# Kernel tuning notes

Measured on AMD Instinct MI355X. Metric: run time of the kernel, lower is better.

The kernel has to match this reference:

```python
import jax, jax.numpy as jnp
import numpy as np

D_MODEL = 1024
NHEAD = 16
EPS = 1e-5


def pos_embed(x, pos):
    # Faithful, vectorized form of the sparse rotation matrix in the source.
    # Source builds rot[..., i, i+1] = sin(pos*i*omega) for even i and
    # rot[..., i, i-1] = cos(pos*i*omega) for odd i, then contracts the feature
    # dim of x against the rotation (intended einsum 'btf,btfd->btd').
    # Resulting column j: even j <- x[..., j+1]*cos(pos*(j+1)*omega),
    #                     odd  j <- x[..., j-1]*sin(pos*(j-1)*omega).
    d = x.shape[-1]
    omega = jnp.pi / d
    i_even = jnp.arange(0, d, 2, dtype=x.dtype)   # even rows -> odd output cols (sin)
    i_odd = jnp.arange(1, d, 2, dtype=x.dtype)    # odd rows  -> even output cols (cos)
    p = pos[..., None]  # (L,B,1)
    sin_part = jnp.sin(p * i_even * omega) * x[..., 0::2]  # -> odd columns
    cos_part = jnp.cos(p * i_odd * omega) * x[..., 1::2]   # -> even columns
    # interleave: even col = cos_part, odd col = sin_part
    return jnp.stack([cos_part, sin_part], axis=-1).reshape(x.shape)


def layer_norm_eps(x, w, b):
    # Source uses torch.var default (unbiased, ddof=1)
    mean = jnp.mean(x, axis=-1, keepdims=True)
    var = jnp.var(x, axis=-1, keepdims=True, ddof=1)
    return w * (x - mean) / jnp.sqrt(var + EPS) + b


def mha(q, k, v, w_qkv, b_qkv, w_o, b_o, nhead):
    L, B, E = q.shape
    S = k.shape[0]
    hd = E // nhead
    wq, wk, wv = jnp.split(w_qkv, 3, axis=0)
    bq, bk, bv = jnp.split(b_qkv, 3, axis=0)
    qp = (q @ wq.T + bq).reshape(L, B, nhead, hd).transpose(1, 2, 0, 3)  # (B,h,L,hd)
    kp = (k @ wk.T + bk).reshape(S, B, nhead, hd).transpose(1, 2, 0, 3)
    vp = (v @ wv.T + bv).reshape(S, B, nhead, hd).transpose(1, 2, 0, 3)
    scale = jnp.asarray(1.0 / np.sqrt(hd), q.dtype)
    scores = jnp.einsum('bhld,bhsd->bhls', qp, kp) * scale
    attn = jax.nn.softmax(scores, axis=-1)
    out = jnp.einsum('bhls,bhsd->bhld', attn, vp)
    out = out.transpose(2, 0, 1, 3).reshape(L, B, E) @ w_o.T + b_o
    ws = attn.mean(axis=1)  # average over heads, torch default
    return out, ws


def setup_inputs() -> dict:
    key = jax.random.key(0)
    ks = jax.random.split(key, 16)
    T, S, B, E, FF = 1024, 1024, 4, D_MODEL, 4096
    sd = 0.02
    return {
        'tgt': jax.random.normal(ks[0], (T, B, E), jnp.float32),
        'memory': jax.random.normal(ks[1], (S, B, E), jnp.float32),
        'pos': jax.random.uniform(ks[2], (S, B), jnp.float32) * S,
        'query_pos': jax.random.uniform(ks[3], (T, B), jnp.float32) * T,
        'w_qkv_self': jax.random.normal(ks[4], (3 * E, E), jnp.float32) * sd,
        'b_qkv_self': jnp.zeros((3 * E,), jnp.float32),
        'w_o_self': jax.random.normal(ks[5], (E, E), jnp.float32) * sd,
        'b_o_self': jnp.zeros((E,), jnp.float32),
        'w_qkv_cross': jax.random.normal(ks[6], (3 * E, E), jnp.float32) * sd,
        'b_qkv_cross': jnp.zeros((3 * E,), jnp.float32),
        'w_o_cross': jax.random.normal(ks[7], (E, E), jnp.float32) * sd,
        'b_o_cross': jnp.zeros((E,), jnp.float32),
        'w1': jax.random.normal(ks[8], (FF, E), jnp.float32) * sd,
        'b1': jnp.zeros((FF,), jnp.float32),
        'w2': jax.random.normal(ks[9], (E, FF), jnp.float32) * sd,
        'b2': jnp.zeros((E,), jnp.float32),
        'g1': jnp.ones((E,), jnp.float32),
        'beta1': jnp.zeros((E,), jnp.float32),
        'g2': jnp.ones((E,), jnp.float32),
        'beta2': jnp.zeros((E,), jnp.float32),
    }


def reference(tgt, memory, pos, query_pos,
              w_qkv_self, b_qkv_self, w_o_self, b_o_self,
              w_qkv_cross, b_qkv_cross, w_o_cross, b_o_cross,
              w1, b1, w2, b2, g1, beta1, g2, beta2):
    # normalize_before=False, residual=True, dropout inactive (eval)
    qk = pos_embed(tgt, query_pos)
    tgt2, _ = mha(qk, qk, tgt, w_qkv_self, b_qkv_self, w_o_self, b_o_self, NHEAD)
    tgt = tgt + tgt2
    tgt = layer_norm_eps(tgt, g1, beta1)
    tgt2, ws = mha(pos_embed(tgt, query_pos), pos_embed(memory, pos), memory,
                   w_qkv_cross, b_qkv_cross, w_o_cross, b_o_cross, NHEAD)
    tgt = tgt + tgt2
    tgt = layer_norm_eps(tgt, g2, beta2)
    tgt2 = jax.nn.relu(tgt @ w1.T + b1) @ w2.T + b2
    tgt = tgt + tgt2
    return tgt, ws
```

## Files before the change

kernel.cpp:

```cpp
#include <hip/hip_runtime.h>

typedef unsigned short u16;
typedef __attribute__((ext_vector_type(8))) short short8;
typedef __attribute__((ext_vector_type(8))) unsigned short u16x8;
typedef __attribute__((ext_vector_type(4))) float f32x4;

#define GLOAD16(SRC, DST) __builtin_amdgcn_global_load_lds( \
    (const __attribute__((address_space(1))) void*)(SRC),   \
    (__attribute__((address_space(3))) void*)(DST), 16, 0, 0)

#define SWZ(BKv, r) ((BKv) == 32 ? (((r) >> 1) & 3) : ((r) & 7))

#define QSCALE 0.18033688011112042f

__device__ __forceinline__ u16 f2bf(float f) {
  union { float f; unsigned u; } v; v.f = f;
  unsigned r = v.u + 0x7fffu + ((v.u >> 16) & 1u);
  return (u16)(r >> 16);
}
__device__ __forceinline__ float bf2f(u16 h) {
  union { unsigned u; float f; } v; v.u = ((unsigned)h) << 16;
  return v.f;
}

__global__ __launch_bounds__(256) void wcvt_kernel(const float* __restrict__ s0,
                                                   const float* __restrict__ s1,
                                                   const float* __restrict__ s2,
                                                   const float* __restrict__ s3,
                                                   const float* __restrict__ s4,
                                                   const float* __restrict__ s5,
                                                   u16* __restrict__ dst) {
  long i = ((long)blockIdx.x * 256 + threadIdx.x) * 4;
  const float* src; long off;
  if (i < 3145728)        { src = s0; off = 0; }
  else if (i < 4194304)   { src = s1; off = 3145728; }
  else if (i < 7340032)   { src = s2; off = 4194304; }
  else if (i < 8388608)   { src = s3; off = 7340032; }
  else if (i < 12582912)  { src = s4; off = 8388608; }
  else                    { src = s5; off = 12582912; }
  float4 v = *(const float4*)(src + (i - off));
  ushort4 o; o.x = f2bf(v.x); o.y = f2bf(v.y); o.z = f2bf(v.z); o.w = f2bf(v.w);
  *(ushort4*)(dst + i) = o;
}

__global__ __launch_bounds__(256) void pos_embed_kernel(const float* __restrict__ x,
                                                        const float* __restrict__ pos,
                                                        u16* __restrict__ out,
                                                        u16* __restrict__ out2,
                                                        u16* __restrict__ raw) {
  int m = blockIdx.x;
  int tid = threadIdx.x;
  float p = pos[m];
  long base = ((long)m << 10);
  int j = tid * 4;
  float4 xv = *(const float4*)(x + base + j);
  const float inv = 1.0f / 2048.0f;
  float r0 = p * (float)(j + 0) * inv;
  float r1 = p * (float)(j + 1) * inv;
  float r2 = p * (float)(j + 2) * inv;
  float r3 = p * (float)(j + 3) * inv;
  float s1 = __builtin_amdgcn_sinf(r0 - floorf(r0));
  float c0 = __builtin_amdgcn_cosf(r1 - floorf(r1));
  float s3 = __builtin_amdgcn_sinf(r2 - floorf(r2));
  float c2 = __builtin_amdgcn_cosf(r3 - floorf(r3));
  ushort4 o;
  o.x = f2bf(c0 * xv.y);
  o.y = f2bf(s1 * xv.x);
  o.z = f2bf(c2 * xv.w);
  o.w = f2bf(s3 * xv.z);
  *(ushort4*)(out + base + j) = o;
  if (out2) *(ushort4*)(out2 + base + j) = o;
  if (raw) {
    ushort4 rw; rw.x = f2bf(xv.x); rw.y = f2bf(xv.y); rw.z = f2bf(xv.z); rw.w = f2bf(xv.w);
    *(ushort4*)(raw + base + j) = rw;
  }
}

__global__ __launch_bounds__(256) void split_qkv_kernel(const u16* __restrict__ P,
                                                        u16* __restrict__ Qb,
                                                        u16* __restrict__ Kb,
                                                        u16* __restrict__ Vtb) {
  long e = ((long)blockIdx.x * 256 + threadIdx.x) * 8;
  int m = (int)(e / 3072);
  int n = (int)(e % 3072);
  int t = m >> 2, b = m & 3;
  int sec = n >> 10, nn = n & 1023;
  int h = nn >> 6, d = nn & 63;
  long bh = b * 16 + h;
  u16x8 v = *(const u16x8*)(P + e);
  if (sec == 0) {
    *(u16x8*)(Qb + (bh << 16) + ((long)t << 6) + d) = v;
  } else if (sec == 1) {
    *(u16x8*)(Kb + (bh << 16) + ((long)t << 6) + d) = v;
  } else {
    u16* dst = Vtb + (bh << 16) + ((long)d << 10) + t;
#pragma unroll
    for (int q = 0; q < 8; q++) dst[(long)q << 10] = v[q];
  }
}

__global__ __launch_bounds__(256) void fattn_kernel(const u16* __restrict__ Q,
                                                    const u16* __restrict__ K,
                                                    const u16* __restrict__ Vt,
                                                    u16* __restrict__ AO,
                                                    float2* __restrict__ Ml) {
  __shared__ u16 lK[2][4096];
  __shared__ u16 lV[2][4096];
  __shared__ u16 lP[4][1024];
  const int tid = threadIdx.x, lane = tid & 63, wid = tid >> 6;
  const int nb = gridDim.x * gridDim.y;
  const int orig = blockIdx.y * gridDim.x + blockIdx.x;
  const int swz = (orig & 7) * (nb >> 3) + (orig >> 3);
  const int qt = swz & 15;
  const int bh = swz >> 4;
  const int b = bh >> 4, h = bh & 15;
  const u16* Qp = Q + ((long)bh << 16);
  const u16* Kp = K + ((long)bh << 16);
  const u16* Vp = Vt + ((long)bh << 16);
  const int q0 = qt << 6;
  const int cr = lane >> 4;

  short8 af0, af1;
  {
    const u16* qs = Qp + (long)(q0 + wid * 16 + (lane & 15)) * 64 + cr * 8;
    af0 = *(const short8*)qs;
    af1 = *(const short8*)(qs + 32);
  }

  float m = -1e30f, l = 0.f;
  f32x4 acco[4] = {};

  auto stage = [&](int bufi, int kv) {
    int s0 = kv << 6;
#pragma unroll
    for (int it = 0; it < 2; it++) {
      int c = it * 256 + tid;
      int row = c >> 3, ch = c & 7;
      int sch = (ch ^ (row & 7)) * 8;
      GLOAD16(Kp + (long)(s0 + row) * 64 + sch, &lK[bufi][c * 8]);
      GLOAD16(Vp + (long)row * 1024 + s0 + sch, &lV[bufi][c * 8]);
    }
  };

  stage(0, 0);
  __syncthreads();
  int buf = 0;
  for (int kv = 0; kv < 16; kv++) {
    if (kv < 15) stage(buf ^ 1, kv + 1);
    f32x4 accs[4];
    __builtin_amdgcn_s_setprio(1);
#pragma unroll
    for (int j = 0; j < 4; j++) {
      int sr = j * 16 + (lane & 15);
      const short8 kf0 = *(const short8*)&lK[buf][sr * 64 + ((cr ^ (sr & 7)) * 8)];
      const short8 kf1 = *(const short8*)&lK[buf][sr * 64 + (((4 + cr) ^ (sr & 7)) * 8)];
      f32x4 zz = {};
      zz = __builtin_amdgcn_mfma_f32_16x16x32_bf16(kf0, af0, zz, 0, 0, 0);
      accs[j] = __builtin_amdgcn_mfma_f32_16x16x32_bf16(kf1, af1, zz, 0, 0, 0);
    }
    __builtin_amdgcn_s_setprio(0);
    float tm = fmaxf(fmaxf(fmaxf(accs[0][0], accs[0][1]), fmaxf(accs[0][2], accs[0][3])),
                     fmaxf(fmaxf(accs[1][0], accs[1][1]), fmaxf(accs[1][2], accs[1][3])));
    float tm2 = fmaxf(fmaxf(fmaxf(accs[2][0], accs[2][1]), fmaxf(accs[2][2], accs[2][3])),
                      fmaxf(fmaxf(accs[3][0], accs[3][1]), fmaxf(accs[3][2], accs[3][3])));
    tm = fmaxf(tm, tm2);
    tm = fmaxf(tm, __shfl_xor(tm, 16));
    tm = fmaxf(tm, __shfl_xor(tm, 32));
    if (!__all(tm - m <= 8.0f)) {
      float mn = fmaxf(m, tm);
      float f = __builtin_amdgcn_exp2f(m - mn);
      m = mn; l *= f;
#pragma unroll
      for (int r = 0; r < 4; r++) {
        float fr = __shfl(f, cr * 4 + r);
        acco[0][r] *= fr; acco[1][r] *= fr; acco[2][r] *= fr; acco[3][r] *= fr;
      }
    }
    float rs = 0.f;
#pragma unroll
    for (int j = 0; j < 4; j++)
#pragma unroll
      for (int r = 0; r < 4; r++) {
        float p = __builtin_amdgcn_exp2f(accs[j][r] - m);
        accs[j][r] = p;
        rs += p;
      }
    rs += __shfl_xor(rs, 16);
    rs += __shfl_xor(rs, 32);
    l += rs;
    {
      u16* pw = lP[wid];
      int q = lane & 15;
      int rowoff = q * 64;
      int qs7 = q & 7;
#pragma unroll
      for (int j = 0; j < 4; j++) {
        uint2 pk;
        asm("v_cvt_pk_bf16_f32 %0, %1, %2"
            : "=v"(pk.x) : "v"(accs[j][0]), "v"(accs[j][1]));
        asm("v_cvt_pk_bf16_f32 %0, %1, %2"
            : "=v"(pk.y) : "v"(accs[j][2]), "v"(accs[j][3]));
        int chunk = 2 * j + (cr >> 1);
        int idx = rowoff + ((chunk ^ qs7) * 8) + 4 * (cr & 1);
        *(uint2*)(pw + idx) = pk;
      }
    }
    {
      int ql = lane & 15;
      const u16* pr = &lP[wid][ql * 64];
      short8 pa0 = *(const short8*)&pr[(cr ^ (ql & 7)) * 8];
      short8 pa1 = *(const short8*)&pr[((4 + cr) ^ (ql & 7)) * 8];
      __builtin_amdgcn_s_setprio(1);
#pragma unroll
      for (int j = 0; j < 4; j++) {
        int dr = j * 16 + (lane & 15);
        const short8 vf0 = *(const short8*)&lV[buf][dr * 64 + ((cr ^ (dr & 7)) * 8)];
        const short8 vf1 = *(const short8*)&lV[buf][dr * 64 + (((4 + cr) ^ (dr & 7)) * 8)];
        acco[j] = __builtin_amdgcn_mfma_f32_16x16x32_bf16(pa0, vf0, acco[j], 0, 0, 0);
        acco[j] = __builtin_amdgcn_mfma_f32_16x16x32_bf16(pa1, vf1, acco[j], 0, 0, 0);
      }
      __builtin_amdgcn_s_setprio(0);
    }
    __syncthreads();
    buf ^= 1;
  }
  float invl = 1.0f / l;
  float ilr[4];
#pragma unroll
  for (int r = 0; r < 4; r++) ilr[r] = __shfl(invl, cr * 4 + r);
#pragma unroll
  for (int j = 0; j < 4; j++)
#pragma unroll
    for (int r = 0; r < 4; r++) {
      int t = q0 + wid * 16 + cr * 4 + r;
      int e = (b << 10) + (h << 6) + j * 16 + (lane & 15);
      AO[(long)t * 4096 + e] = f2bf(acco[j][r] * ilr[r]);
    }
  if (Ml && lane < 16) {
    int t = q0 + wid * 16 + lane;
    Ml[((long)bh << 10) + t] = make_float2(m, invl);
  }
}

__global__ __launch_bounds__(256) void wsrec_kernel(const u16* __restrict__ Q,
                                                    const u16* __restrict__ K,
                                                    const float2* __restrict__ Ml,
                                                    float* __restrict__ ws) {
  __shared__ u16 lK[2][4096];
  const int tid = threadIdx.x, lane = tid & 63, wid = tid >> 6;
  const int nb = gridDim.x * gridDim.y;
  const int orig = blockIdx.y * gridDim.x + blockIdx.x;
  const int swz = (orig & 7) * (nb >> 3) + (orig >> 3);
  const int st = swz & 15, lt = swz >> 4;
  const int b = blockIdx.z;
  const int s0 = st << 6, l0 = lt << 6;
  const int cr = lane >> 4;

  auto stage = [&](int bufi, int h) {
    const u16* Kp = K + (((long)(b * 16 + h)) << 16);
#pragma unroll
    for (int it = 0; it < 2; it++) {
      int c = it * 256 + tid;
      int row = c >> 3, ch = c & 7;
      GLOAD16(Kp + (long)(s0 + row) * 64 + ((ch ^ (row & 7)) * 8), &lK[bufi][c * 8]);
    }
  };

  f32x4 wacc[4] = {};
  stage(0, 0);
  __syncthreads();
  int buf = 0;
  for (int h = 0; h < 16; h++) {
    if (h < 15) stage(buf ^ 1, h + 1);
    const int bh = b * 16 + h;
    short8 af0, af1;
    {
      const u16* qs = Q + ((long)bh << 16) + (long)(l0 + wid * 16 + (lane & 15)) * 64 + cr * 8;
      af0 = *(const short8*)qs;
      af1 = *(const short8*)(qs + 32);
    }
    f32x4 accs[4];
    __builtin_amdgcn_s_setprio(1);
#pragma unroll
    for (int j = 0; j < 4; j++) {
      int sr = j * 16 + (lane & 15);
      const short8 kf0 = *(const short8*)&lK[buf][sr * 64 + ((cr ^ (sr & 7)) * 8)];
      const short8 kf1 = *(const short8*)&lK[buf][sr * 64 + (((4 + cr) ^ (sr & 7)) * 8)];
      f32x4 zz = {};
      zz = __builtin_amdgcn_mfma_f32_16x16x32_bf16(af0, kf0, zz, 0, 0, 0);
      accs[j] = __builtin_amdgcn_mfma_f32_16x16x32_bf16(af1, kf1, zz, 0, 0, 0);
    }
    __builtin_amdgcn_s_setprio(0);
    float mm[4], il[4];
#pragma unroll
    for (int r = 0; r < 4; r++) {
      float2 v = Ml[((long)bh << 10) + l0 + wid * 16 + (lane >> 4) * 4 + r];
      mm[r] = v.x; il[r] = v.y * 0.0625f;
    }
#pragma unroll
    for (int j = 0; j < 4; j++)
#pragma unroll
      for (int r = 0; r < 4; r++)
        wacc[j][r] += __builtin_amdgcn_exp2f(accs[j][r] - mm[r]) * il[r];
    __syncthreads();
    buf ^= 1;
  }
#pragma unroll
  for (int j = 0; j < 4; j++)
#pragma unroll
    for (int r = 0; r < 4; r++) {
      int li = l0 + wid * 16 + (lane >> 4) * 4 + r;
      int si = s0 + j * 16 + (lane & 15);
      ws[((long)b << 20) + (long)li * 1024 + si] = wacc[j][r];
    }
}

__global__ __launch_bounds__(256) void ln_kernel(const float* __restrict__ X,
                                                 const float* __restrict__ D1,
                                                 const float* __restrict__ D2,
                                                 const float* __restrict__ bo,
                                                 const float* __restrict__ g,
                                                 const float* __restrict__ be,
                                                 float* __restrict__ out,
                                                 u16* __restrict__ bfout) {
  int mrow = blockIdx.x;
  int tid = threadIdx.x, lane = tid & 63, wid = tid >> 6;
  long base = ((long)mrow << 10);
  float4 a = *(const float4*)(X + base + tid * 4);
  float4 b = *(const float4*)(D1 + base + tid * 4);
  float x0 = a.x + b.x, x1 = a.y + b.y, x2 = a.z + b.z, x3 = a.w + b.w;
  if (D2) {
    float4 c = *(const float4*)(D2 + base + tid * 4);
    x0 += c.x; x1 += c.y; x2 += c.z; x3 += c.w;
  }
  if (bo) {
    float4 c = *(const float4*)(bo + tid * 4);
    x0 += c.x; x1 += c.y; x2 += c.z; x3 += c.w;
  }
  float s = x0 + x1 + x2 + x3;
#pragma unroll
  for (int o = 32; o; o >>= 1) s += __shfl_xor(s, o);
  __shared__ float red[4];
  if (lane == 0) red[wid] = s;
  __syncthreads();
  float mean = (red[0] + red[1] + red[2] + red[3]) * (1.0f / 1024.0f);
  float d0 = x0 - mean, d1 = x1 - mean, d2 = x2 - mean, d3 = x3 - mean;
  float ss = d0 * d0 + d1 * d1 + d2 * d2 + d3 * d3;
#pragma unroll
  for (int o = 32; o; o >>= 1) ss += __shfl_xor(ss, o);
  __syncthreads();
  if (lane == 0) red[wid] = ss;
  __syncthreads();
  float var = (red[0] + red[1] + red[2] + red[3]) * (1.0f / 1023.0f);
  float sc = 1.0f / sqrtf(var + 1e-5f);
  float4 gv = *(const float4*)(g + tid * 4);
  float4 bv = *(const float4*)(be + tid * 4);
  float y0 = gv.x * d0 * sc + bv.x;
  float y1 = gv.y * d1 * sc + bv.y;
  float y2 = gv.z * d2 * sc + bv.z;
  float y3 = gv.w * d3 * sc + bv.w;
  float4 o4; o4.x = y0; o4.y = y1; o4.z = y2; o4.w = y3;
  *(float4*)(out + base + tid * 4) = o4;
  if (bfout) {
    ushort4 hh; hh.x = f2bf(y0); hh.y = f2bf(y1); hh.z = f2bf(y2); hh.w = f2bf(y3);
    *(ushort4*)(bfout + base + tid * 4) = hh;
  }
}

__global__ __launch_bounds__(256) void add3_kernel(const float* __restrict__ X,
                                                   const float* __restrict__ P0,
                                                   const float* __restrict__ P1,
                                                   const float* __restrict__ b,
                                                   float* __restrict__ out) {
  long i = ((long)blockIdx.x * 256 + threadIdx.x) * 4;
  int col = (int)(i & 1023);
  float4 x = *(const float4*)(X + i);
  float4 p = *(const float4*)(P0 + i);
  float4 q = *(const float4*)(P1 + i);
  float4 bb = *(const float4*)(b + col);
  float4 o;
  o.x = x.x + p.x + q.x + bb.x;
  o.y = x.y + p.y + q.y + bb.y;
  o.z = x.z + p.z + q.z + bb.z;
  o.w = x.w + p.w + q.w + bb.w;
  *(float4*)(out + i) = o;
}

template <int BM, int BN, int BK, int WR, int WC, int NT, int DB>
__global__ __launch_bounds__(NT)
void gemm_bt_kernel(const u16* __restrict__ A, const u16* __restrict__ B,
                    void* __restrict__ C, const float* __restrict__ bias,
                    int lda, int ldb, int ldc, int K,
                    long sAz, long sBz, long sCz, long sbz,
                    float alpha, int flags) {
  constexpr int WTM = BM / WR, WTN = BN / WC;
  constexpr int FM = WTM / 16, FN = WTN / 16;
  constexpr int NC = BK / 8;
  __shared__ u16 lA[DB][BM * BK];
  __shared__ u16 lB[DB][BN * BK];
  const int tid = threadIdx.x, lane = tid & 63, wid = tid >> 6;
  const int wr = wid / WC, wc = wid % WC;
  const int z = blockIdx.z;

  const int nwg = gridDim.x * gridDim.y;
  const int orig = blockIdx.y * gridDim.x + blockIdx.x;
  const int qq = nwg >> 3, rr = nwg & 7;
  const int xcd = orig & 7, idx = orig >> 3;
  const int swz = (xcd < rr ? xcd * (qq + 1) : rr * (qq + 1) + (xcd - rr) * qq) + idx;
  const int bxs = swz % gridDim.x;
  const int bys = swz / gridDim.x;

  const u16* Ab = A + z * sAz + (long)bys * BM * lda;
  const u16* Bb = B + z * sBz + (long)bxs * BN * ldb;

  f32x4 acc[FM][FN] = {};

  auto stage = [&](int bufi, int k0) {
#pragma unroll
    for (int c0 = 0; c0 < BM * NC; c0 += NT) {
      int c = c0 + tid;
      if ((BM * NC) % NT == 0 || c < BM * NC) {
        int row = c / NC, ch = c % NC;
        int sch = ch ^ SWZ(BK, row);
        GLOAD16(Ab + (long)row * lda + k0 + sch * 8, &lA[bufi][c * 8]);
      }
    }
#pragma unroll
    for (int c0 = 0; c0 < BN * NC; c0 += NT) {
      int c = c0 + tid;
      if ((BN * NC) % NT == 0 || c < BN * NC) {
        int row = c / NC, ch = c % NC;
        int sch = ch ^ SWZ(BK, row);
        GLOAD16(Bb + (long)row * ldb + k0 + sch * 8, &lB[bufi][c * 8]);
      }
    }
  };

  auto compute = [&](int bufi) {
#pragma unroll
    for (int kk = 0; kk < BK / 32; kk++) {
      short8 afv[FM], bfv[FN];
#pragma unroll
      for (int i = 0; i < FM; i++) {
        int row = wr * WTM + i * 16 + (lane & 15);
        int ch = kk * 4 + (lane >> 4);
        afv[i] = *(const short8*)&lA[bufi][row * BK + ((ch ^ SWZ(BK, row)) * 8)];
      }
#pragma unroll
      for (int j = 0; j < FN; j++) {
        int row = wc * WTN + j * 16 + (lane & 15);
        int ch = kk * 4 + (lane >> 4);
        bfv[j] = *(const short8*)&lB[bufi][row * BK + ((ch ^ SWZ(BK, row)) * 8)];
      }
#pragma unroll
      for (int i = 0; i < FM; i++)
#pragma unroll
        for (int j = 0; j < FN; j++)
          acc[i][j] = __builtin_amdgcn_mfma_f32_16x16x32_bf16(afv[i], bfv[j], acc[i][j], 0, 0, 0);
    }
  };

  const int nk = K / BK;
  if (DB == 2) {
    stage(0, 0);
    __syncthreads();
    int cur = 0;
    for (int t = 0; t < nk; t++) {
      if (t + 1 < nk) stage(cur ^ 1, (t + 1) * BK);
      compute(cur);
      __syncthreads();
      cur ^= 1;
    }
  } else {
    for (int t = 0; t < nk; t++) {
      stage(0, t * BK);
      __syncthreads();
      compute(0);
      __syncthreads();
    }
  }

  const long rbase = (long)bys * BM + wr * WTM;
  const int cbase = bxs * BN + wc * WTN;
  const float* bz = bias ? (bias + z * sbz) : nullptr;
#pragma unroll
  for (int i = 0; i < FM; i++)
#pragma unroll
    for (int j = 0; j < FN; j++)
#pragma unroll
      for (int r = 0; r < 4; r++) {
        long row = rbase + i * 16 + ((lane >> 4) * 4 + r);
        int col = cbase + j * 16 + (lane & 15);
        float v = acc[i][j][r];
        if (!(flags & 8)) v *= alpha;
        if (flags & 1) v += bz[col];
        if ((flags & 8) && z == 0) v *= alpha;
        if (flags & 2) v = fmaxf(v, 0.0f);
        long off = (long)z * sCz + row * (long)ldc + col;
        if (flags & 4) ((float*)C)[off] = v;
        else ((u16*)C)[off] = f2bf(v);
      }
}

extern "C" void kernel_launch(void* const* d_in, const int* in_sizes, int n_in,
                              void* d_out, int out_size, void* d_ws, size_t ws_size,
                              hipStream_t stream) {
  const float* tgt  = (const float*)d_in[0];
  const float* mem  = (const float*)d_in[1];
  const float* pos  = (const float*)d_in[2];
  const float* qpos = (const float*)d_in[3];
  const float* wqkvS = (const float*)d_in[4];
  const float* bqkvS = (const float*)d_in[5];
  const float* woS   = (const float*)d_in[6];
  const float* boS   = (const float*)d_in[7];
  const float* wqkvC = (const float*)d_in[8];
  const float* bqkvC = (const float*)d_in[9];
  const float* woC   = (const float*)d_in[10];
  const float* boC   = (const float*)d_in[11];
  const float* w1  = (const float*)d_in[12];
  const float* b1  = (const float*)d_in[13];
  const float* w2  = (const float*)d_in[14];
  const float* b2  = (const float*)d_in[15];
  const float* g1  = (const float*)d_in[16];
  const float* be1 = (const float*)d_in[17];
  const float* g2  = (const float*)d_in[18];
  const float* be2 = (const float*)d_in[19];

  const size_t MB = 1024ull * 1024ull;
  float* out0 = (float*)d_out;
  float* wsout = out0 + 4194304;

  char* W = (char*)d_ws;
  u16* wb = (u16*)W;
  u16* wqkvS_b = wb;
  u16* woS_b   = wb + 3145728;
  u16* wqkvC_b = wb + 4194304;
  u16* woC_b   = wb + 7340032;
  u16* w1_b    = wb + 8388608;
  u16* w2_b    = wb + 12582912;
  float* Xf   = (float*)(W + 32 * MB);
  float* OPar = (float*)(W + 48 * MB);
  u16* Pq  = (u16*)(W + 48 * MB);
  u16* bf1 = (u16*)(W + 80 * MB);
  u16* bf2 = (u16*)(W + 88 * MB);
  u16* bf3 = (u16*)(W + 96 * MB);
  float2* Ml = (float2*)(W + 96 * MB);
  u16* Qb  = (u16*)(W + 104 * MB);
  u16* Kb  = (u16*)(W + 112 * MB);
  u16* Vtb = (u16*)(W + 120 * MB);
  u16* AOb = (u16*)(W + 128 * MB);
  u16* F1  = (u16*)(W + 104 * MB);

  wcvt_kernel<<<16384, 256, 0, stream>>>(wqkvS, woS, wqkvC, woC, w1, w2, wb);

  pos_embed_kernel<<<4096, 256, 0, stream>>>(tgt, qpos, bf1, bf2, bf3);
  gemm_bt_kernel<128, 128, 64, 2, 4, 512, 2><<<dim3(8, 32, 3), 512, 0, stream>>>(
      bf1, wqkvS_b, Pq, bqkvS, 1024, 1024, 3072, 1024,
      4194304, 1048576, 1024, 1024, QSCALE, 1 | 8);
  split_qkv_kernel<<<6144, 256, 0, stream>>>(Pq, Qb, Kb, Vtb);
  fattn_kernel<<<dim3(16, 64), 256, 0, stream>>>(Qb, Kb, Vtb, AOb, nullptr);
  gemm_bt_kernel<128, 128, 32, 2, 4, 512, 2><<<dim3(8, 32, 2), 512, 0, stream>>>(
      AOb, woS_b, OPar, nullptr, 1024, 1024, 1024, 512,
      512, 512, 4194304, 0, 1.0f, 4);
  ln_kernel<<<4096, 256, 0, stream>>>(tgt, OPar, OPar + 4194304, boS, g1, be1, Xf, nullptr);

  pos_embed_kernel<<<4096, 256, 0, stream>>>(Xf, qpos, bf1, nullptr, nullptr);
  pos_embed_kernel<<<4096, 256, 0, stream>>>(mem, pos, bf2, nullptr, bf3);
  gemm_bt_kernel<128, 128, 64, 2, 4, 512, 2><<<dim3(8, 32, 3), 512, 0, stream>>>(
      bf1, wqkvC_b, Pq, bqkvC, 1024, 1024, 3072, 1024,
      4194304, 1048576, 1024, 1024, QSCALE, 1 | 8);
  split_qkv_kernel<<<6144, 256, 0, stream>>>(Pq, Qb, Kb, Vtb);
  fattn_kernel<<<dim3(16, 64), 256, 0, stream>>>(Qb, Kb, Vtb, AOb, Ml);
  wsrec_kernel<<<dim3(16, 16, 4), 256, 0, stream>>>(Qb, Kb, Ml, wsout);
  gemm_bt_kernel<128, 128, 32, 2, 4, 512, 2><<<dim3(8, 32, 2), 512, 0, stream>>>(
      AOb, woC_b, OPar, nullptr, 1024, 1024, 1024, 512,
      512, 512, 4194304, 0, 1.0f, 4);
  ln_kernel<<<4096, 256, 0, stream>>>(Xf, OPar, OPar + 4194304, boC, g2, be2, Xf, bf1);

  gemm_bt_kernel<128, 128, 64, 2, 4, 512, 2><<<dim3(32, 32, 1), 512, 0, stream>>>(
      bf1, w1_b, F1, b1, 1024, 1024, 4096, 1024, 0, 0, 0, 0, 1.0f, 1 | 2);
  gemm_bt_kernel<128, 128, 64, 2, 4, 512, 2><<<dim3(8, 32, 2), 512, 0, stream>>>(
      F1, w2_b, OPar, nullptr, 4096, 4096, 1024, 2048,
      2048, 2048, 4194304, 0, 1.0f, 4);
  add3_kernel<<<4096, 256, 0, stream>>>(Xf, OPar, OPar + 4194304, b2, out0);
}
```

Baseline: 448.6 us.

## Fuse QKV head split into GEMM epilogue and pos-embed into layernorm

The QKV projection GEMM now writes Q, K and transposed V directly in per-head layout through a new epilogue flag, so both split_qkv launches and the intermediate Pq buffer go away. The first layernorm now applies the query positional rotation while producing its bf16 output, which removes a separate pos_embed launch and a re-read of Xf. Several GEMMs also move from a BK of 64 to 32. The direct per-head writes, especially the transposed V stores, are scattered rather than row-contiguous, which could hurt store efficiency. The smaller K tile changes pipeline depth and the number of LDS barriers per GEMM.

```diff
diff --git a/kernel.cpp b/kernel.cpp
--- a/kernel.cpp
+++ b/kernel.cpp
@@ -76,29 +76,6 @@
   }
 }
 
-__global__ __launch_bounds__(256) void split_qkv_kernel(const u16* __restrict__ P,
-                                                        u16* __restrict__ Qb,
-                                                        u16* __restrict__ Kb,
-                                                        u16* __restrict__ Vtb) {
-  long e = ((long)blockIdx.x * 256 + threadIdx.x) * 8;
-  int m = (int)(e / 3072);
-  int n = (int)(e % 3072);
-  int t = m >> 2, b = m & 3;
-  int sec = n >> 10, nn = n & 1023;
-  int h = nn >> 6, d = nn & 63;
-  long bh = b * 16 + h;
-  u16x8 v = *(const u16x8*)(P + e);
-  if (sec == 0) {
-    *(u16x8*)(Qb + (bh << 16) + ((long)t << 6) + d) = v;
-  } else if (sec == 1) {
-    *(u16x8*)(Kb + (bh << 16) + ((long)t << 6) + d) = v;
-  } else {
-    u16* dst = Vtb + (bh << 16) + ((long)d << 10) + t;
-#pragma unroll
-    for (int q = 0; q < 8; q++) dst[(long)q << 10] = v[q];
-  }
-}
-
 __global__ __launch_bounds__(256) void fattn_kernel(const u16* __restrict__ Q,
                                                     const u16* __restrict__ K,
                                                     const u16* __restrict__ Vt,
@@ -322,7 +299,8 @@
                                                  const float* __restrict__ g,
                                                  const float* __restrict__ be,
                                                  float* __restrict__ out,
-                                                 u16* __restrict__ bfout) {
+                                                 u16* __restrict__ bfout,
+                                                 const float* __restrict__ pepos) {
   int mrow = blockIdx.x;
   int tid = threadIdx.x, lane = tid & 63, wid = tid >> 6;
   long base = ((long)mrow << 10);
@@ -362,7 +340,26 @@
   float4 o4; o4.x = y0; o4.y = y1; o4.z = y2; o4.w = y3;
   *(float4*)(out + base + tid * 4) = o4;
   if (bfout) {
-    ushort4 hh; hh.x = f2bf(y0); hh.y = f2bf(y1); hh.z = f2bf(y2); hh.w = f2bf(y3);
+    ushort4 hh;
+    if (pepos) {
+      float p = pepos[mrow];
+      int j = tid * 4;
+      const float inv = 1.0f / 2048.0f;
+      float r0 = p * (float)(j + 0) * inv;
+      float r1 = p * (float)(j + 1) * inv;
+      float r2 = p * (float)(j + 2) * inv;
+      float r3 = p * (float)(j + 3) * inv;
+      float s1 = __builtin_amdgcn_sinf(r0 - floorf(r0));
+      float c0 = __builtin_amdgcn_cosf(r1 - floorf(r1));
+      float s3 = __builtin_amdgcn_sinf(r2 - floorf(r2));
+      float c2 = __builtin_amdgcn_cosf(r3 - floorf(r3));
+      hh.x = f2bf(c0 * y1);
+      hh.y = f2bf(s1 * y0);
+      hh.z = f2bf(c2 * y3);
+      hh.w = f2bf(s3 * y2);
+    } else {
+      hh.x = f2bf(y0); hh.y = f2bf(y1); hh.z = f2bf(y2); hh.w = f2bf(y3);
+    }
     *(ushort4*)(bfout + base + tid * 4) = hh;
   }
 }
@@ -461,7 +458,7 @@
   };
 
   const int nk = K / BK;
-  if (DB == 2) {
+  if constexpr (DB == 2) {
     stage(0, 0);
     __syncthreads();
     int cur = 0;
@@ -496,9 +493,18 @@
         if (flags & 1) v += bz[col];
         if ((flags & 8) && z == 0) v *= alpha;
         if (flags & 2) v = fmaxf(v, 0.0f);
-        long off = (long)z * sCz + row * (long)ldc + col;
-        if (flags & 4) ((float*)C)[off] = v;
-        else ((u16*)C)[off] = f2bf(v);
+        if (flags & 16) {
+          int t = (int)(row >> 2), bb = (int)(row & 3);
+          int hh = col >> 6, dd = col & 63;
+          long base16 = ((long)(bb * 16 + hh)) << 16;
+          long off = (long)z * 4194304 + base16 +
+                     (z == 2 ? (long)dd * 1024 + t : (long)t * 64 + dd);
+          ((u16*)C)[off] = f2bf(v);
+        } else {
+          long off = (long)z * sCz + row * (long)ldc + col;
+          if (flags & 4) ((float*)C)[off] = v;
+          else ((u16*)C)[off] = f2bf(v);
+        }
       }
 }
 
@@ -540,7 +546,6 @@
   u16* w2_b    = wb + 12582912;
   float* Xf   = (float*)(W + 32 * MB);
   float* OPar = (float*)(W + 48 * MB);
-  u16* Pq  = (u16*)(W + 48 * MB);
   u16* bf1 = (u16*)(W + 80 * MB);
   u16* bf2 = (u16*)(W + 88 * MB);
   u16* bf3 = (u16*)(W + 96 * MB);
@@ -554,32 +559,31 @@
   wcvt_kernel<<<16384, 256, 0, stream>>>(wqkvS, woS, wqkvC, woC, w1, w2, wb);
 
   pos_embed_kernel<<<4096, 256, 0, stream>>>(tgt, qpos, bf1, bf2, bf3);
-  gemm_bt_kernel<128, 128, 64, 2, 4, 512, 2><<<dim3(8, 32, 3), 512, 0, stream>>>(
-      bf1, wqkvS_b, Pq, bqkvS, 1024, 1024, 3072, 1024,
-      4194304, 1048576, 1024, 1024, QSCALE, 1 | 8);
-  split_qkv_kernel<<<6144, 256, 0, stream>>>(Pq, Qb, Kb, Vtb);
+  gemm_bt_kernel<128, 128, 32, 2, 4, 512, 2><<<dim3(8, 32, 3), 512, 0, stream>>>(
+      bf1, wqkvS_b, Qb, bqkvS, 1024, 1024, 0, 1024,
+      4194304, 1048576, 0, 1024, QSCALE, 1 | 8 | 16);
   fattn_kernel<<<dim3(16, 64), 256, 0, stream>>>(Qb, Kb, Vtb, AOb, nullptr);
   gemm_bt_kernel<128, 128, 32, 2, 4, 512, 2><<<dim3(8, 32, 2), 512, 0, stream>>>(
       AOb, woS_b, OPar, nullptr, 1024, 1024, 1024, 512,
       512, 512, 4194304, 0, 1.0f, 4);
-  ln_kernel<<<4096, 256, 0, stream>>>(tgt, OPar, OPar + 4194304, boS, g1, be1, Xf, nullptr);
-
-  pos_embed_kernel<<<4096, 256, 0, stream>>>(Xf, qpos, bf1, nullptr, nullptr);
+  ln_kernel<<<4096, 256, 0, stream>>>(tgt, OPar, OPar + 4194304, boS, g1, be1,
+                                      Xf, bf1, qpos);
+
   pos_embed_kernel<<<4096, 256, 0, stream>>>(mem, pos, bf2, nullptr, bf3);
-  gemm_bt_kernel<128, 128, 64, 2, 4, 512, 2><<<dim3(8, 32, 3), 512, 0, stream>>>(
-      bf1, wqkvC_b, Pq, bqkvC, 1024, 1024, 3072, 1024,
-      4194304, 1048576, 1024, 1024, QSCALE, 1 | 8);
-  split_qkv_kernel<<<6144, 256, 0, stream>>>(Pq, Qb, Kb, Vtb);
+  gemm_bt_kernel<128, 128, 32, 2, 4, 512, 2><<<dim3(8, 32, 3), 512, 0, stream>>>(
+      bf1, wqkvC_b, Qb, bqkvC, 1024, 1024, 0, 1024,
+      4194304, 1048576, 0, 1024, QSCALE, 1 | 8 | 16);
   fattn_kernel<<<dim3(16, 64), 256, 0, stream>>>(Qb, Kb, Vtb, AOb, Ml);
   wsrec_kernel<<<dim3(16, 16, 4), 256, 0, stream>>>(Qb, Kb, Ml, wsout);
   gemm_bt_kernel<128, 128, 32, 2, 4, 512, 2><<<dim3(8, 32, 2), 512, 0, stream>>>(
       AOb, woC_b, OPar, nullptr, 1024, 1024, 1024, 512,
       512, 512, 4194304, 0, 1.0f, 4);
-  ln_kernel<<<4096, 256, 0, stream>>>(Xf, OPar, OPar + 4194304, boC, g2, be2, Xf, bf1);
-
-  gemm_bt_kernel<128, 128, 64, 2, 4, 512, 2><<<dim3(32, 32, 1), 512, 0, stream>>>(
+  ln_kernel<<<4096, 256, 0, stream>>>(Xf, OPar, OPar + 4194304, boC, g2, be2,
+                                      Xf, bf1, nullptr);
+
+  gemm_bt_kernel<128, 128, 32, 2, 4, 512, 2><<<dim3(32, 32, 1), 512, 0, stream>>>(
       bf1, w1_b, F1, b1, 1024, 1024, 4096, 1024, 0, 0, 0, 0, 1.0f, 1 | 2);
-  gemm_bt_kernel<128, 128, 64, 2, 4, 512, 2><<<dim3(8, 32, 2), 512, 0, stream>>>(
+  gemm_bt_kernel<128, 128, 32, 2, 4, 512, 2><<<dim3(8, 32, 2), 512, 0, stream>>>(
       F1, w2_b, OPar, nullptr, 4096, 4096, 1024, 2048,
       2048, 2048, 4194304, 0, 1.0f, 4);
   add3_kernel<<<4096, 256, 0, stream>>>(Xf, OPar, OPar + 4194304, b2, out0);
```

New measurement: 403.2 us. 10.1% less time.
